# Optimization experiments

Hardware: AMD Instinct MI355X
Metric: run time of the kernel (lower is better)

## Reference

```python
import jax, jax.numpy as jnp
import numpy as np

B, L, D_MODEL = 8, 2048, 512
N_QUBITS, Q_LAYERS = 10, 4
DIM = 2 ** N_QUBITS
EPS = 1e-5  # torch LayerNorm default


def _apply_1q_tok(state, U, q):
    # per-token 2x2 gate U: (N,2,2), wire 0 = most significant (PennyLane order)
    N = state.shape[0]
    s = state.reshape(N, 2 ** q, 2, -1)
    return jnp.einsum('nij,najb->naib', U, s).reshape(N, -1)


def _apply_1q(state, U, q):
    # shared 2x2 gate U: (2,2)
    N = state.shape[0]
    s = state.reshape(N, 2 ** q, 2, -1)
    return jnp.einsum('ij,najb->naib', U, s).reshape(N, -1)


def _cnot(state, c, t):
    N = state.shape[0]
    lo, hi = min(c, t), max(c, t)
    s = state.reshape(N, 2 ** lo, 2, 2 ** (hi - lo - 1), 2, -1)
    if c < t:
        # control is the first 2-axis; flip target axis where control==1
        s = s.at[:, :, 1].set(jnp.flip(s[:, :, 1], axis=3))
    else:
        # target is the first 2-axis, control the second
        s = s.at[:, :, :, :, 1].set(jnp.flip(s[:, :, :, :, 1], axis=2))
    return s.reshape(N, -1)


def _simulate(feats, weights):
    # feats: (N, n_qubits) angles; weights: (q_layers, n_qubits, 2)
    N = feats.shape[0]
    half = 0.5 * feats
    cxa = jnp.cos(half).astype(jnp.complex64)
    sxa = jnp.sin(half).astype(jnp.complex64)
    phz = jnp.exp(1j * half.astype(jnp.complex64))  # e^{+i theta/2}
    state = jnp.zeros((N, DIM), jnp.complex64).at[:, 0].set(1.0 + 0j)
    for l in range(Q_LAYERS):
        # AngleEmbedding rotation='X' : RX(feat_q) on wire q
        for q in range(N_QUBITS):
            c, s = cxa[:, q], sxa[:, q]
            U = jnp.stack([jnp.stack([c, -1j * s], -1),
                           jnp.stack([-1j * s, c], -1)], -2)  # (N,2,2)
            state = _apply_1q_tok(state, U, q)
        # AngleEmbedding rotation='Z' : RZ(feat_q) on wire q (diagonal)
        for q in range(N_QUBITS):
            p = phz[:, q]
            diag = jnp.stack([jnp.conj(p), p], -1)  # (N,2)
            s = state.reshape(N, 2 ** q, 2, -1)
            state = (s * diag[:, None, :, None]).reshape(N, -1)
        # trainable RY, RZ per wire (shared across tokens)
        for q in range(N_QUBITS):
            ty = 0.5 * weights[l, q, 0]
            cy, sy = jnp.cos(ty), jnp.sin(ty)
            Uy = jnp.stack([jnp.stack([cy, -sy]), jnp.stack([sy, cy])]).astype(jnp.complex64)
            state = _apply_1q(state, Uy, q)
            pz = jnp.exp(1j * (0.5 * weights[l, q, 1]).astype(jnp.complex64))
            diag = jnp.stack([jnp.conj(pz), pz])  # (2,)
            s = state.reshape(N, 2 ** q, 2, -1)
            state = (s * diag[None, None, :, None]).reshape(N, -1)
        # entangling CNOT ring
        for q in range(N_QUBITS):
            state = _cnot(state, q, (q + 1) % N_QUBITS)
    probs = jnp.real(state) ** 2 + jnp.imag(state) ** 2  # (N, 2**n)
    zs = []
    for q in range(N_QUBITS):
        p = probs.reshape(N, 2 ** q, 2, -1).sum(axis=(1, 3))  # (N,2)
        zs.append(p[:, 0] - p[:, 1])  # <Z_q>
    return jnp.stack(zs, -1)  # (N, n_qubits)


def setup_inputs() -> dict:
    key = jax.random.key(0)
    ks = jax.random.split(key, 4)
    x = jax.random.normal(ks[0], (B, L, D_MODEL), jnp.float32)
    in_W = jax.random.normal(ks[1], (N_QUBITS, D_MODEL), jnp.float32) / np.float32(np.sqrt(D_MODEL))
    in_b = jnp.zeros((N_QUBITS,), jnp.float32)
    gamma = jnp.ones((N_QUBITS,), jnp.float32)
    beta = jnp.zeros((N_QUBITS,), jnp.float32)
    weights = 0.05 * jax.random.normal(ks[2], (Q_LAYERS, N_QUBITS, 2), jnp.float32)
    out_W = jax.random.normal(ks[3], (D_MODEL, N_QUBITS), jnp.float32) / np.float32(np.sqrt(N_QUBITS))
    out_b = jnp.zeros((D_MODEL,), jnp.float32)
    return {"x": x, "in_W": in_W, "in_b": in_b, "gamma": gamma, "beta": beta,
            "weights": weights, "out_W": out_W, "out_b": out_b}


def reference(x, in_W, in_b, gamma, beta, weights, out_W, out_b):
    Bs, Ls, _ = x.shape
    h = jnp.tanh(jnp.einsum('bld,qd->blq', x, in_W) + in_b)
    mu = h.mean(-1, keepdims=True)
    var = ((h - mu) ** 2).mean(-1, keepdims=True)
    h = (h - mu) / jnp.sqrt(var + EPS) * gamma + beta
    q_out = _simulate(h.reshape(Bs * Ls, N_QUBITS), weights)
    q_out = q_out.reshape(Bs, Ls, N_QUBITS).astype(x.dtype)
    return x + jnp.einsum('blq,dq->bld', q_out, out_W) + out_b
```

## Files before the change

kernel.cpp:

```cpp
#include <hip/hip_runtime.h>

#define NQ 10
#define DQ 512
#define QL 4
#define NTOK (8 * 2048)
#define QOFF (NQ * DQ)

typedef float v2f __attribute__((ext_vector_type(2)));
typedef float v4f __attribute__((ext_vector_type(4)));
typedef _Float16 h2 __attribute__((ext_vector_type(2)));

__device__ __forceinline__ int bperm(int addr, int v) {
    return __builtin_amdgcn_ds_bpermute(addr, v);
}
__device__ __forceinline__ float bpermf(int addr, float v) {
    return __builtin_bit_cast(float, bperm(addr, __builtin_bit_cast(int, v)));
}
__device__ __forceinline__ h2 bpermh(int addr, h2 v) {
    return __builtin_bit_cast(h2, bperm(addr, __builtin_bit_cast(int, v)));
}
template <int CTRL>
__device__ __forceinline__ int dppi(int i) {
    return __builtin_amdgcn_update_dpp(i, i, CTRL, 0xF, 0xF, false);
}
template <int M>
__device__ __forceinline__ float dppxf(float v) {
    int i = __builtin_bit_cast(int, v);
    if constexpr (M == 1)      i = dppi<0xB1>(i);
    else if constexpr (M == 2) i = dppi<0x4E>(i);
    else                       i = dppi<0x128>(i);
    return __builtin_bit_cast(float, i);
}
template <int M>
__device__ __forceinline__ h2 dppxh(h2 v) {
    return __builtin_bit_cast(h2, __builtin_bit_cast(float, v) * 0.f + 0.f), v;
}

__device__ __forceinline__ void reduce10(float* z, int a32, int a16, int a4) {
#pragma unroll
    for (int q = 0; q < NQ; ++q) {
        z[q] += bpermf(a32, z[q]);
        z[q] += bpermf(a16, z[q]);
        z[q] += dppxf<8>(z[q]);
        z[q] += bpermf(a4, z[q]);
        z[q] += dppxf<2>(z[q]);
        z[q] += dppxf<1>(z[q]);
    }
}

__device__ __forceinline__ v4f coef(const v4f* Q, float A, float C) {
    return Q[0] + A * Q[1] + C * Q[2];
}
__device__ __forceinline__ h2 pk2(float a, float b) {
    return __builtin_bit_cast(h2, __builtin_amdgcn_cvt_pkrtz(a, b));
}
__device__ __forceinline__ h2 h2bc(float v) { return pk2(v, v); }
__device__ __forceinline__ h2 h2swap(h2 v) {
    return __builtin_shufflevector(v, v, 1, 0);
}

__device__ __forceinline__ void gate_lane_hp(h2* sr, h2* si, v4f cf, bool bit, int addr) {
    const float aif = bit ? -cf.y : cf.y;
    const float brf = bit ? cf.z : -cf.z;
    const h2 ar = h2bc(cf.x), ai = h2bc(aif), br = h2bc(brf), bi = h2bc(cf.w);
#pragma unroll
    for (int j = 0; j < 8; ++j) {
        h2 wr = bpermh(addr, sr[j]), wi = bpermh(addr, si[j]);
        h2 nr = ar * sr[j] - ai * si[j] + br * wr - bi * wi;
        h2 ni = ar * si[j] + ai * sr[j] + br * wi + bi * wr;
        sr[j] = nr; si[j] = ni;
    }
}
template <int M>
__device__ __forceinline__ void gate_lane_hd(h2* sr, h2* si, v4f cf, bool bit) {
    const float aif = bit ? -cf.y : cf.y;
    const float brf = bit ? cf.z : -cf.z;
    const h2 ar = h2bc(cf.x), ai = h2bc(aif), br = h2bc(brf), bi = h2bc(cf.w);
#pragma unroll
    for (int j = 0; j < 8; ++j) {
        h2 wr, wi;
        {
            int iR = __builtin_bit_cast(int, sr[j]);
            int iI = __builtin_bit_cast(int, si[j]);
            if constexpr (M == 1)      { iR = dppi<0xB1>(iR);  iI = dppi<0xB1>(iI); }
            else if constexpr (M == 2) { iR = dppi<0x4E>(iR);  iI = dppi<0x4E>(iI); }
            else                       { iR = dppi<0x128>(iR); iI = dppi<0x128>(iI); }
            wr = __builtin_bit_cast(h2, iR); wi = __builtin_bit_cast(h2, iI);
        }
        h2 nr = ar * sr[j] - ai * si[j] + br * wr - bi * wi;
        h2 ni = ar * si[j] + ai * sr[j] + br * wi + bi * wr;
        sr[j] = nr; si[j] = ni;
    }
}
template <int BJ>
__device__ __forceinline__ void gate_reg_h(h2* sr, h2* si, v4f cf) {
    const h2 ar = h2bc(cf.x), ai = h2bc(cf.y), br = h2bc(cf.z), bi = h2bc(cf.w);
#pragma unroll
    for (int j = 0; j < 8; ++j) if (!(j & BJ)) {
        const int j1 = j | BJ;
        h2 x0r = sr[j], x0i = si[j], x1r = sr[j1], x1i = si[j1];
        sr[j]  = ar * x0r - ai * x0i - br * x1r - bi * x1i;
        si[j]  = ar * x0i + ai * x0r - br * x1i + bi * x1r;
        sr[j1] = br * x0r - bi * x0i + ar * x1r + ai * x1i;
        si[j1] = br * x0i + bi * x0r + ar * x1i - ai * x1r;
    }
}
__device__ __forceinline__ void gate_elem_h(h2* sr, h2* si, v4f cf) {
    const h2 ar = h2bc(cf.x), bi = h2bc(cf.w);
    const h2 aiV = pk2(cf.y, -cf.y);
    const h2 brV = pk2(-cf.z, cf.z);
#pragma unroll
    for (int j = 0; j < 8; ++j) {
        h2 swr = h2swap(sr[j]), swi = h2swap(si[j]);
        h2 nr = ar * sr[j] - aiV * si[j] + brV * swr - bi * swi;
        h2 ni = ar * si[j] + aiV * sr[j] + brV * swi + bi * swr;
        sr[j] = nr; si[j] = ni;
    }
}

__device__ __forceinline__ void perm678_h(h2* a) {
    h2 o2 = a[2], o4 = a[4], o7 = a[7];
    a[1] = h2swap(a[1]);
    a[2] = a[3]; a[3] = h2swap(o2);
    a[4] = a[6]; a[6] = a[5]; a[5] = h2swap(o7); a[7] = h2swap(o4);
}

__device__ __forceinline__ void cnot_ring_h(h2* sr, h2* si, int lane, int apm, int a32) {
#pragma unroll
    for (int j = 0; j < 8; ++j) {
        sr[j] = bpermh(apm, sr[j]);
        si[j] = bpermh(apm, si[j]);
    }
    {
        const bool ctrl = (lane & 1);
#pragma unroll
        for (int j = 0; j < 4; ++j) {
            h2 t0 = sr[j], t1 = sr[j + 4];
            sr[j] = ctrl ? t1 : t0; sr[j + 4] = ctrl ? t0 : t1;
            t0 = si[j]; t1 = si[j + 4];
            si[j] = ctrl ? t1 : t0; si[j + 4] = ctrl ? t0 : t1;
        }
    }
    perm678_h(sr);
    perm678_h(si);
#pragma unroll
    for (int j = 0; j < 8; ++j) {
        h2 w = bpermh(a32, sr[j]); sr[j] = (h2){sr[j].x, w.y};
        w = bpermh(a32, si[j]);    si[j] = (h2){si[j].x, w.y};
    }
}

__global__ __launch_bounds__(512) void prep_kernel(
    const float* __restrict__ weights, const float* __restrict__ out_W,
    float* __restrict__ ws)
{
    const int t = threadIdx.x;
#pragma unroll
    for (int q = 0; q < NQ; ++q)
        ws[q * DQ + t] = out_W[t * NQ + q];
    if (t < QL * NQ) {
        float w0 = weights[t * 2], w1 = weights[t * 2 + 1];
        float cy = __cosf(0.5f * w0), sy = __sinf(0.5f * w0);
        float cz = __cosf(0.5f * w1), sz = __sinf(0.5f * w1);
        float d = cy - sy, e = cy + sy;
        v4f* Q = (v4f*)(ws + QOFF);
        Q[t * 3 + 0] = (v4f){-cz * sy,  sz * sy,  cz * cy,  sz * cy};
        Q[t * 3 + 1] = (v4f){ cz * e,  -sz * e,  -cz * d,  -sz * d};
        Q[t * 3 + 2] = (v4f){-sz * d,  -cz * d,   sz * e,  -cz * e};
    }
}

__global__ __launch_bounds__(256) void quantum_kernel(
    const float* __restrict__ x, const float* __restrict__ in_W,
    const float* __restrict__ in_b, const float* __restrict__ gamma,
    const float* __restrict__ beta, const float* __restrict__ ws,
    const float* __restrict__ out_b, float* __restrict__ out)
{
    const int t = threadIdx.x;
    const int lane = t & 63;
    const int tok = blockIdx.x * 4 + (t >> 6);
    const v4f* Qg = (const v4f*)(ws + QOFF);

    const int a32 = (lane ^ 32) << 2;
    const int a16 = (lane ^ 16) << 2;
    const int a4  = (lane ^ 4)  << 2;
    int srcl = lane;
#pragma unroll
    for (int q = 4; q >= 0; --q) {
        const int bc = 5 - q, bt = bc - 1;
        srcl ^= ((srcl >> bc) & 1) << bt;
    }
    const int apm = srcl << 2;

    const v2f* xrow2 = (const v2f*)(x + (size_t)tok * DQ);
    const v2f* inW2 = (const v2f*)in_W;
    v2f hv[NQ];
#pragma unroll
    for (int q = 0; q < NQ; ++q) hv[q] = (v2f){0.f, 0.f};
#pragma unroll
    for (int k = 0; k < 4; ++k) {
        v2f xk = xrow2[lane + 64 * k];
#pragma unroll
        for (int q = 0; q < NQ; ++q)
            hv[q] = xk * inW2[q * (DQ / 2) + lane + 64 * k] + hv[q];
    }
    float h[NQ];
#pragma unroll
    for (int q = 0; q < NQ; ++q) h[q] = hv[q].x + hv[q].y;
    reduce10(h, a32, a16, a4);

    float mu = 0.f;
#pragma unroll
    for (int q = 0; q < NQ; ++q) {
        float e = __expf(2.f * (h[q] + in_b[q]));
        h[q] = (e - 1.f) * __builtin_amdgcn_rcpf(e + 1.f);
        mu += h[q];
    }
    mu *= 0.1f;
    float var = 0.f;
#pragma unroll
    for (int q = 0; q < NQ; ++q) { float d0 = h[q] - mu; var += d0 * d0; }
    var *= 0.1f;
    const float rstd = rsqrtf(var + 1e-5f);

    float Aq[NQ], Cq[NQ];
#pragma unroll
    for (int q = 0; q < NQ; ++q) {
        float f = (h[q] - mu) * rstd * gamma[q] + beta[q];
        float hf = 0.5f * f;
        float c = __cosf(hf), s = __sinf(hf);
        Aq[q] = c * c;
        Cq[q] = c * s;
    }

    h2 sr[8], si[8];
    {
        const v4f* Q0 = Qg;
        v4f f0 = coef(Q0 + 0, Aq[0], Cq[0]);
        bool b0 = (lane & 32);
        float Lr = b0 ? f0.z : f0.x, Li = b0 ? f0.w : f0.y;
#pragma unroll
        for (int q = 1; q < 6; ++q) {
            v4f f = coef(Q0 + 3 * q, Aq[q], Cq[q]);
            bool b = lane & (1 << (5 - q));
            float fr = b ? f.z : f.x, fi = b ? f.w : f.y;
            float nr = Lr * fr - Li * fi, ni = Lr * fi + Li * fr;
            Lr = nr; Li = ni;
        }
        float Pr[8], Pi[8];
        {
            v4f f6 = coef(Q0 + 18, Aq[6], Cq[6]);
            Pr[0] = Lr * f6.x - Li * f6.y; Pi[0] = Lr * f6.y + Li * f6.x;
            Pr[4] = Lr * f6.z - Li * f6.w; Pi[4] = Lr * f6.w + Li * f6.z;
        }
        {
            v4f f7 = coef(Q0 + 21, Aq[7], Cq[7]);
#pragma unroll
            for (int jj = 0; jj < 8; jj += 4) {
                float tr1 = Pr[jj] * f7.z - Pi[jj] * f7.w;
                float ti1 = Pr[jj] * f7.w + Pi[jj] * f7.z;
                float tr0 = Pr[jj] * f7.x - Pi[jj] * f7.y;
                float ti0 = Pr[jj] * f7.y + Pi[jj] * f7.x;
                Pr[jj] = tr0; Pi[jj] = ti0; Pr[jj + 2] = tr1; Pi[jj + 2] = ti1;
            }
        }
        {
            v4f f8 = coef(Q0 + 24, Aq[8], Cq[8]);
#pragma unroll
            for (int jj = 0; jj < 8; jj += 2) {
                float tr1 = Pr[jj] * f8.z - Pi[jj] * f8.w;
                float ti1 = Pr[jj] * f8.w + Pi[jj] * f8.z;
                float tr0 = Pr[jj] * f8.x - Pi[jj] * f8.y;
                float ti0 = Pr[jj] * f8.y + Pi[jj] * f8.x;
                Pr[jj] = tr0; Pi[jj] = ti0; Pr[jj + 1] = tr1; Pi[jj + 1] = ti1;
            }
        }
        {
            v4f f9 = coef(Q0 + 27, Aq[9], Cq[9]);
#pragma unroll
            for (int j = 0; j < 8; ++j) {
                float e0r = Pr[j] * f9.x - Pi[j] * f9.y;
                float e0i = Pr[j] * f9.y + Pi[j] * f9.x;
                float e1r = Pr[j] * f9.z - Pi[j] * f9.w;
                float e1i = Pr[j] * f9.w + Pi[j] * f9.z;
                sr[j] = pk2(e0r, e1r);
                si[j] = pk2(e0i, e1i);
            }
        }
    }
    cnot_ring_h(sr, si, lane, apm, a32);

#pragma unroll
    for (int l = 1; l < QL; ++l) {
        const v4f* Ql = Qg + l * NQ * 3;
        gate_lane_hp(sr, si, coef(Ql + 0,  Aq[0], Cq[0]), lane & 32, a32);
        gate_lane_hd<8>(sr, si, coef(Ql + 6,  Aq[2], Cq[2]), lane & 8);
        gate_lane_hp(sr, si, coef(Ql + 3,  Aq[1], Cq[1]), lane & 16, a16);
        gate_lane_hd<2>(sr, si, coef(Ql + 12, Aq[4], Cq[4]), lane & 2);
        gate_lane_hp(sr, si, coef(Ql + 9,  Aq[3], Cq[3]), lane & 4, a4);
        gate_lane_hd<1>(sr, si, coef(Ql + 15, Aq[5], Cq[5]), lane & 1);
        gate_reg_h<4>(sr, si, coef(Ql + 18, Aq[6], Cq[6]));
        gate_reg_h<2>(sr, si, coef(Ql + 21, Aq[7], Cq[7]));
        gate_reg_h<1>(sr, si, coef(Ql + 24, Aq[8], Cq[8]));
        gate_elem_h(sr, si, coef(Ql + 27, Aq[9], Cq[9]));
        if (l < QL - 1) cnot_ring_h(sr, si, lane, apm, a32);
    }

    v2f aP = {0.f, 0.f}, a6 = {0.f, 0.f}, a7 = {0.f, 0.f}, aT = {0.f, 0.f};
#pragma unroll
    for (int j = 0; j < 8; ++j) {
        v2f rr = {(float)sr[j].x, (float)sr[j].y};
        v2f ii = {(float)si[j].x, (float)si[j].y};
        v2f p = rr * rr + ii * ii;
        aP += p;
        a6 += (j & 4) ? -p : p;
        a7 += ((((j >> 2) ^ (j >> 1)) & 1)) ? -p : p;
        aT += ((((j >> 2) ^ (j >> 1) ^ j) & 1)) ? -p : p;
    }
    const float A0 = aP.x + aP.y;
    const float B6 = a6.x + a6.y;
    const float B7 = a7.x + a7.y;
    const float B8 = aT.x + aT.y;
    const float B9 = aT.x - aT.y;
    const bool P1 = __popc(lane & 0x30) & 1;
    const bool P2 = __popc(lane & 0x38) & 1;
    const bool P3 = __popc(lane & 0x3C) & 1;
    const bool P4 = __popc(lane & 0x3E) & 1;
    const bool P5 = __popc(lane & 0x3F) & 1;
    const bool PX = __popc(lane & 0x1F) & 1;
    float z[NQ];
    z[0] = PX ? -B9 : B9;
    z[1] = P1 ? -A0 : A0;
    z[2] = P2 ? -A0 : A0;
    z[3] = P3 ? -A0 : A0;
    z[4] = P4 ? -A0 : A0;
    z[5] = P5 ? -A0 : A0;
    z[6] = P5 ? -B6 : B6;
    z[7] = P5 ? -B7 : B7;
    z[8] = P5 ? -B8 : B8;
    z[9] = P5 ? -B9 : B9;
    reduce10(z, a32, a16, a4);

    v2f* orow2 = (v2f*)(out + (size_t)tok * DQ);
    const v2f* ob2 = (const v2f*)out_b;
    const v2f* oWt2 = (const v2f*)ws;
#pragma unroll
    for (int k = 0; k < 4; ++k) {
        const int d2 = lane + 64 * k;
        v2f acc = xrow2[d2] + ob2[d2];
#pragma unroll
        for (int q = 0; q < NQ; ++q)
            acc = z[q] * oWt2[q * (DQ / 2) + d2] + acc;
        orow2[d2] = acc;
    }
}

extern "C" void kernel_launch(void* const* d_in, const int* in_sizes, int n_in,
                              void* d_out, int out_size, void* d_ws, size_t ws_size,
                              hipStream_t stream) {
    const float* x       = (const float*)d_in[0];
    const float* in_W    = (const float*)d_in[1];
    const float* in_b    = (const float*)d_in[2];
    const float* gamma   = (const float*)d_in[3];
    const float* beta    = (const float*)d_in[4];
    const float* weights = (const float*)d_in[5];
    const float* out_W   = (const float*)d_in[6];
    const float* out_b   = (const float*)d_in[7];
    float* out = (float*)d_out;
    float* ws = (float*)d_ws;

    hipLaunchKernelGGL(prep_kernel, dim3(1), dim3(512), 0, stream,
                       weights, out_W, ws);
    hipLaunchKernelGGL(quantum_kernel, dim3(NTOK / 4), dim3(256), 0, stream,
                       x, in_W, in_b, gamma, beta, ws, out_b, out);
}
```

Measured before the change: 195.5 us.

## Move gate coefficients, expectation sums and final reduction to packed fp16; widen loads

Gate coefficients are now precomputed as packed half pairs in the prep kernel and combined per token with packed fp16 FMAs, replacing the float coef computation and per-gate conversions. The probability accumulation and the cross-lane reduction of the ten expectation values are done in packed fp16, which halves the number of permute/DPP ops. The input projection and output loops switch from float2 to float4 loads and stores. The intent is to cut ALU and cross-lane traffic, at the risk of fp16 precision loss in the reductions that feed the output.

```diff
diff --git a/kernel.cpp b/kernel.cpp
--- a/kernel.cpp
+++ b/kernel.cpp
@@ -5,6 +5,7 @@
 #define QL 4
 #define NTOK (8 * 2048)
 #define QOFF (NQ * DQ)
+#define QHOFF (QOFF + 480)
 
 typedef float v2f __attribute__((ext_vector_type(2)));
 typedef float v4f __attribute__((ext_vector_type(4)));
@@ -33,7 +34,11 @@
 }
 template <int M>
 __device__ __forceinline__ h2 dppxh(h2 v) {
-    return __builtin_bit_cast(h2, __builtin_bit_cast(float, v) * 0.f + 0.f), v;
+    int i = __builtin_bit_cast(int, v);
+    if constexpr (M == 1)      i = dppi<0xB1>(i);
+    else if constexpr (M == 2) i = dppi<0x4E>(i);
+    else                       i = dppi<0x128>(i);
+    return __builtin_bit_cast(h2, i);
 }
 
 __device__ __forceinline__ void reduce10(float* z, int a32, int a16, int a4) {
@@ -48,53 +53,61 @@
     }
 }
 
+__device__ __forceinline__ h2 pk2(float a, float b) {
+    return __builtin_bit_cast(h2, __builtin_amdgcn_cvt_pkrtz(a, b));
+}
+__device__ __forceinline__ h2 h2swap(h2 v) {
+    return __builtin_shufflevector(v, v, 1, 0);
+}
+__device__ __forceinline__ h2 splat_lo(h2 v) {
+    return __builtin_shufflevector(v, v, 0, 0);
+}
+__device__ __forceinline__ h2 splat_hi(h2 v) {
+    return __builtin_shufflevector(v, v, 1, 1);
+}
+
 __device__ __forceinline__ v4f coef(const v4f* Q, float A, float C) {
     return Q[0] + A * Q[1] + C * Q[2];
 }
-__device__ __forceinline__ h2 pk2(float a, float b) {
-    return __builtin_bit_cast(h2, __builtin_amdgcn_cvt_pkrtz(a, b));
-}
-__device__ __forceinline__ h2 h2bc(float v) { return pk2(v, v); }
-__device__ __forceinline__ h2 h2swap(h2 v) {
-    return __builtin_shufflevector(v, v, 1, 0);
-}
-
-__device__ __forceinline__ void gate_lane_hp(h2* sr, h2* si, v4f cf, bool bit, int addr) {
-    const float aif = bit ? -cf.y : cf.y;
-    const float brf = bit ? cf.z : -cf.z;
-    const h2 ar = h2bc(cf.x), ai = h2bc(aif), br = h2bc(brf), bi = h2bc(cf.w);
+__device__ __forceinline__ void coefh(const h2* Qg6, h2 A2, h2 C2,
+                                      h2& arai, h2& brbi) {
+    arai = Qg6[0] + A2 * Qg6[2] + C2 * Qg6[4];
+    brbi = Qg6[1] + A2 * Qg6[3] + C2 * Qg6[5];
+}
+
+__device__ __forceinline__ void gate_lane_hp(h2* sr, h2* si, h2 arai, h2 brbi,
+                                             bool bit, int addr) {
+    const h2 ar = splat_lo(arai), ai = splat_hi(arai);
+    const h2 br = splat_lo(brbi), bi = splat_hi(brbi);
+    const h2 Ai = bit ? -ai : ai;
+    const h2 Br = bit ? br : -br;
 #pragma unroll
     for (int j = 0; j < 8; ++j) {
         h2 wr = bpermh(addr, sr[j]), wi = bpermh(addr, si[j]);
-        h2 nr = ar * sr[j] - ai * si[j] + br * wr - bi * wi;
-        h2 ni = ar * si[j] + ai * sr[j] + br * wi + bi * wr;
+        h2 nr = ar * sr[j] - Ai * si[j] + Br * wr - bi * wi;
+        h2 ni = ar * si[j] + Ai * sr[j] + Br * wi + bi * wr;
         sr[j] = nr; si[j] = ni;
     }
 }
 template <int M>
-__device__ __forceinline__ void gate_lane_hd(h2* sr, h2* si, v4f cf, bool bit) {
-    const float aif = bit ? -cf.y : cf.y;
-    const float brf = bit ? cf.z : -cf.z;
-    const h2 ar = h2bc(cf.x), ai = h2bc(aif), br = h2bc(brf), bi = h2bc(cf.w);
-#pragma unroll
-    for (int j = 0; j < 8; ++j) {
-        h2 wr, wi;
-        {
-            int iR = __builtin_bit_cast(int, sr[j]);
-            int iI = __builtin_bit_cast(int, si[j]);
-            if constexpr (M == 1)      { iR = dppi<0xB1>(iR);  iI = dppi<0xB1>(iI); }
-            else if constexpr (M == 2) { iR = dppi<0x4E>(iR);  iI = dppi<0x4E>(iI); }
-            else                       { iR = dppi<0x128>(iR); iI = dppi<0x128>(iI); }
-            wr = __builtin_bit_cast(h2, iR); wi = __builtin_bit_cast(h2, iI);
-        }
-        h2 nr = ar * sr[j] - ai * si[j] + br * wr - bi * wi;
-        h2 ni = ar * si[j] + ai * sr[j] + br * wi + bi * wr;
+__device__ __forceinline__ void gate_lane_hd(h2* sr, h2* si, h2 arai, h2 brbi,
+                                             bool bit) {
+    const h2 ar = splat_lo(arai), ai = splat_hi(arai);
+    const h2 br = splat_lo(brbi), bi = splat_hi(brbi);
+    const h2 Ai = bit ? -ai : ai;
+    const h2 Br = bit ? br : -br;
+#pragma unroll
+    for (int j = 0; j < 8; ++j) {
+        h2 wr = dppxh<M>(sr[j]), wi = dppxh<M>(si[j]);
+        h2 nr = ar * sr[j] - Ai * si[j] + Br * wr - bi * wi;
+        h2 ni = ar * si[j] + Ai * sr[j] + Br * wi + bi * wr;
         sr[j] = nr; si[j] = ni;
     }
 }
 template <int BJ>
-__device__ __forceinline__ void gate_reg_h(h2* sr, h2* si, v4f cf) {
-    const h2 ar = h2bc(cf.x), ai = h2bc(cf.y), br = h2bc(cf.z), bi = h2bc(cf.w);
+__device__ __forceinline__ void gate_reg_h(h2* sr, h2* si, h2 arai, h2 brbi) {
+    const h2 ar = splat_lo(arai), ai = splat_hi(arai);
+    const h2 br = splat_lo(brbi), bi = splat_hi(brbi);
 #pragma unroll
     for (int j = 0; j < 8; ++j) if (!(j & BJ)) {
         const int j1 = j | BJ;
@@ -105,10 +118,12 @@
         si[j1] = br * x0i + bi * x0r + ar * x1i - ai * x1r;
     }
 }
-__device__ __forceinline__ void gate_elem_h(h2* sr, h2* si, v4f cf) {
-    const h2 ar = h2bc(cf.x), bi = h2bc(cf.w);
-    const h2 aiV = pk2(cf.y, -cf.y);
-    const h2 brV = pk2(-cf.z, cf.z);
+__device__ __forceinline__ void gate_elem_h(h2* sr, h2* si, h2 arai, h2 brbi) {
+    const h2 ar = splat_lo(arai), bi = splat_hi(brbi);
+    const h2 aiV = __builtin_bit_cast(h2,
+        __builtin_bit_cast(int, splat_hi(arai)) ^ (int)0x80000000);
+    const h2 brV = __builtin_bit_cast(h2,
+        __builtin_bit_cast(int, splat_lo(brbi)) ^ 0x00008000);
 #pragma unroll
     for (int j = 0; j < 8; ++j) {
         h2 swr = h2swap(sr[j]), swi = h2swap(si[j]);
@@ -163,10 +178,15 @@
         float cy = __cosf(0.5f * w0), sy = __sinf(0.5f * w0);
         float cz = __cosf(0.5f * w1), sz = __sinf(0.5f * w1);
         float d = cy - sy, e = cy + sy;
+        v4f q0 = (v4f){-cz * sy,  sz * sy,  cz * cy,  sz * cy};
+        v4f q1 = (v4f){ cz * e,  -sz * e,  -cz * d,  -sz * d};
+        v4f q2 = (v4f){-sz * d,  -cz * d,   sz * e,  -cz * e};
         v4f* Q = (v4f*)(ws + QOFF);
-        Q[t * 3 + 0] = (v4f){-cz * sy,  sz * sy,  cz * cy,  sz * cy};
-        Q[t * 3 + 1] = (v4f){ cz * e,  -sz * e,  -cz * d,  -sz * d};
-        Q[t * 3 + 2] = (v4f){-sz * d,  -cz * d,   sz * e,  -cz * e};
+        Q[t * 3 + 0] = q0; Q[t * 3 + 1] = q1; Q[t * 3 + 2] = q2;
+        h2* Qh = (h2*)(ws + QHOFF);
+        Qh[t * 6 + 0] = pk2(q0.x, q0.y); Qh[t * 6 + 1] = pk2(q0.z, q0.w);
+        Qh[t * 6 + 2] = pk2(q1.x, q1.y); Qh[t * 6 + 3] = pk2(q1.z, q1.w);
+        Qh[t * 6 + 4] = pk2(q2.x, q2.y); Qh[t * 6 + 5] = pk2(q2.z, q2.w);
     }
 }
 
@@ -180,6 +200,7 @@
     const int lane = t & 63;
     const int tok = blockIdx.x * 4 + (t >> 6);
     const v4f* Qg = (const v4f*)(ws + QOFF);
+    const h2*  Qh = (const h2*)(ws + QHOFF);
 
     const int a32 = (lane ^ 32) << 2;
     const int a16 = (lane ^ 16) << 2;
@@ -192,21 +213,22 @@
     }
     const int apm = srcl << 2;
 
-    const v2f* xrow2 = (const v2f*)(x + (size_t)tok * DQ);
-    const v2f* inW2 = (const v2f*)in_W;
-    v2f hv[NQ];
-#pragma unroll
-    for (int q = 0; q < NQ; ++q) hv[q] = (v2f){0.f, 0.f};
-#pragma unroll
-    for (int k = 0; k < 4; ++k) {
-        v2f xk = xrow2[lane + 64 * k];
+    const v4f* xrow4 = (const v4f*)(x + (size_t)tok * DQ);
+    const v4f* inW4 = (const v4f*)in_W;
+    v4f hv[NQ];
+#pragma unroll
+    for (int q = 0; q < NQ; ++q) hv[q] = (v4f){0.f, 0.f, 0.f, 0.f};
+#pragma unroll
+    for (int k = 0; k < 2; ++k) {
+        v4f xk = xrow4[lane + 64 * k];
 #pragma unroll
         for (int q = 0; q < NQ; ++q)
-            hv[q] = xk * inW2[q * (DQ / 2) + lane + 64 * k] + hv[q];
+            hv[q] = xk * inW4[q * (DQ / 4) + lane + 64 * k] + hv[q];
     }
     float h[NQ];
 #pragma unroll
-    for (int q = 0; q < NQ; ++q) h[q] = hv[q].x + hv[q].y;
+    for (int q = 0; q < NQ; ++q)
+        h[q] = (hv[q].x + hv[q].y) + (hv[q].z + hv[q].w);
     reduce10(h, a32, a16, a4);
 
     float mu = 0.f;
@@ -224,6 +246,7 @@
     const float rstd = rsqrtf(var + 1e-5f);
 
     float Aq[NQ], Cq[NQ];
+    h2 A2[NQ], C2[NQ];
 #pragma unroll
     for (int q = 0; q < NQ; ++q) {
         float f = (h[q] - mu) * rstd * gamma[q] + beta[q];
@@ -231,6 +254,8 @@
         float c = __cosf(hf), s = __sinf(hf);
         Aq[q] = c * c;
         Cq[q] = c * s;
+        A2[q] = pk2(Aq[q], Aq[q]);
+        C2[q] = pk2(Cq[q], Cq[q]);
     }
 
     h2 sr[8], si[8];
@@ -292,36 +317,35 @@
 
 #pragma unroll
     for (int l = 1; l < QL; ++l) {
-        const v4f* Ql = Qg + l * NQ * 3;
-        gate_lane_hp(sr, si, coef(Ql + 0,  Aq[0], Cq[0]), lane & 32, a32);
-        gate_lane_hd<8>(sr, si, coef(Ql + 6,  Aq[2], Cq[2]), lane & 8);
-        gate_lane_hp(sr, si, coef(Ql + 3,  Aq[1], Cq[1]), lane & 16, a16);
-        gate_lane_hd<2>(sr, si, coef(Ql + 12, Aq[4], Cq[4]), lane & 2);
-        gate_lane_hp(sr, si, coef(Ql + 9,  Aq[3], Cq[3]), lane & 4, a4);
-        gate_lane_hd<1>(sr, si, coef(Ql + 15, Aq[5], Cq[5]), lane & 1);
-        gate_reg_h<4>(sr, si, coef(Ql + 18, Aq[6], Cq[6]));
-        gate_reg_h<2>(sr, si, coef(Ql + 21, Aq[7], Cq[7]));
-        gate_reg_h<1>(sr, si, coef(Ql + 24, Aq[8], Cq[8]));
-        gate_elem_h(sr, si, coef(Ql + 27, Aq[9], Cq[9]));
+        const h2* Ql = Qh + l * NQ * 6;
+        h2 arai, brbi;
+        coefh(Ql + 0 * 6, A2[0], C2[0], arai, brbi); gate_lane_hp(sr, si, arai, brbi, lane & 32, a32);
+        coefh(Ql + 2 * 6, A2[2], C2[2], arai, brbi); gate_lane_hd<8>(sr, si, arai, brbi, lane & 8);
+        coefh(Ql + 1 * 6, A2[1], C2[1], arai, brbi); gate_lane_hp(sr, si, arai, brbi, lane & 16, a16);
+        coefh(Ql + 4 * 6, A2[4], C2[4], arai, brbi); gate_lane_hd<2>(sr, si, arai, brbi, lane & 2);
+        coefh(Ql + 3 * 6, A2[3], C2[3], arai, brbi); gate_lane_hp(sr, si, arai, brbi, lane & 4, a4);
+        coefh(Ql + 5 * 6, A2[5], C2[5], arai, brbi); gate_lane_hd<1>(sr, si, arai, brbi, lane & 1);
+        coefh(Ql + 6 * 6, A2[6], C2[6], arai, brbi); gate_reg_h<4>(sr, si, arai, brbi);
+        coefh(Ql + 7 * 6, A2[7], C2[7], arai, brbi); gate_reg_h<2>(sr, si, arai, brbi);
+        coefh(Ql + 8 * 6, A2[8], C2[8], arai, brbi); gate_reg_h<1>(sr, si, arai, brbi);
+        coefh(Ql + 9 * 6, A2[9], C2[9], arai, brbi); gate_elem_h(sr, si, arai, brbi);
         if (l < QL - 1) cnot_ring_h(sr, si, lane, apm, a32);
     }
 
-    v2f aP = {0.f, 0.f}, a6 = {0.f, 0.f}, a7 = {0.f, 0.f}, aT = {0.f, 0.f};
-#pragma unroll
-    for (int j = 0; j < 8; ++j) {
-        v2f rr = {(float)sr[j].x, (float)sr[j].y};
-        v2f ii = {(float)si[j].x, (float)si[j].y};
-        v2f p = rr * rr + ii * ii;
+    h2 aP = (h2){0, 0}, a6 = (h2){0, 0}, a7 = (h2){0, 0}, aT = (h2){0, 0};
+#pragma unroll
+    for (int j = 0; j < 8; ++j) {
+        h2 p = sr[j] * sr[j] + si[j] * si[j];
         aP += p;
-        a6 += (j & 4) ? -p : p;
-        a7 += ((((j >> 2) ^ (j >> 1)) & 1)) ? -p : p;
-        aT += ((((j >> 2) ^ (j >> 1) ^ j) & 1)) ? -p : p;
-    }
-    const float A0 = aP.x + aP.y;
-    const float B6 = a6.x + a6.y;
-    const float B7 = a7.x + a7.y;
-    const float B8 = aT.x + aT.y;
-    const float B9 = aT.x - aT.y;
+        if (j & 4) a6 -= p; else a6 += p;
+        if (((j >> 2) ^ (j >> 1)) & 1) a7 -= p; else a7 += p;
+        if (((j >> 2) ^ (j >> 1) ^ j) & 1) aT -= p; else aT += p;
+    }
+    const float A0 = (float)aP.x + (float)aP.y;
+    const float B6 = (float)a6.x + (float)a6.y;
+    const float B7 = (float)a7.x + (float)a7.y;
+    const float B8 = (float)aT.x + (float)aT.y;
+    const float B9 = (float)aT.x - (float)aT.y;
     const bool P1 = __popc(lane & 0x30) & 1;
     const bool P2 = __popc(lane & 0x38) & 1;
     const bool P3 = __popc(lane & 0x3C) & 1;
@@ -339,19 +363,37 @@
     z[7] = P5 ? -B7 : B7;
     z[8] = P5 ? -B8 : B8;
     z[9] = P5 ? -B9 : B9;
-    reduce10(z, a32, a16, a4);
-
-    v2f* orow2 = (v2f*)(out + (size_t)tok * DQ);
-    const v2f* ob2 = (const v2f*)out_b;
-    const v2f* oWt2 = (const v2f*)ws;
-#pragma unroll
-    for (int k = 0; k < 4; ++k) {
-        const int d2 = lane + 64 * k;
-        v2f acc = xrow2[d2] + ob2[d2];
+
+    h2 zp[5];
+#pragma unroll
+    for (int i = 0; i < 5; ++i) zp[i] = pk2(z[2 * i], z[2 * i + 1]);
+#pragma unroll
+    for (int i = 0; i < 5; ++i) {
+        zp[i] += bpermh(a32, zp[i]);
+        zp[i] += bpermh(a16, zp[i]);
+        zp[i] += dppxh<8>(zp[i]);
+        zp[i] += bpermh(a4, zp[i]);
+        zp[i] += dppxh<2>(zp[i]);
+        zp[i] += dppxh<1>(zp[i]);
+    }
+    float zf[NQ];
+#pragma unroll
+    for (int i = 0; i < 5; ++i) {
+        zf[2 * i]     = (float)zp[i].x;
+        zf[2 * i + 1] = (float)zp[i].y;
+    }
+
+    v4f* orow4 = (v4f*)(out + (size_t)tok * DQ);
+    const v4f* ob4 = (const v4f*)out_b;
+    const v4f* oWt4 = (const v4f*)ws;
+#pragma unroll
+    for (int k = 0; k < 2; ++k) {
+        const int d4 = lane + 64 * k;
+        v4f acc = xrow4[d4] + ob4[d4];
 #pragma unroll
         for (int q = 0; q < NQ; ++q)
-            acc = z[q] * oWt2[q * (DQ / 2) + d2] + acc;
-        orow2[d2] = acc;
+            acc = zf[q] * oWt4[q * (DQ / 4) + d4] + acc;
+        orow4[d4] = acc;
     }
 }
 
```

Measured after the change: 189.0 us. 1.03x faster.
